# Performance work log

Hardware: AMD Instinct MI355X
Metric: run time of the kernel (lower is better)

The kernel has to match this reference:

```python
import jax, jax.numpy as jnp
import numpy as np
from math import sqrt


def _build_transitions(dim):
    # Upper-triangular (i<=j) pairs in the same row-major order as the torch loop.
    iu0, iu1 = np.triu_indices(dim)
    n_mono = len(iu0)
    idx = np.arange(n_mono)
    M = np.zeros((dim, dim), dtype=np.int32)
    M[iu0, iu1] = idx
    M[iu1, iu0] = idx
    coef_trans = np.full((n_mono, 1), sqrt(2.0), dtype=np.float32)
    coef_trans[idx[iu0 == iu1]] = 1.0  # diagonal coefficients stay scale 1
    return iu0, iu1, M.reshape(-1), coef_trans


def setup_inputs() -> dict:
    key = jax.random.key(0)
    k1, k2, k3, k4 = jax.random.split(key, 4)
    dim, n_quadrics, B = 512, 64, 2048
    n_mono = dim * (dim - 1) // 2 + dim  # 131328
    points = jax.random.normal(k1, (B, dim), dtype=jnp.float32)
    # orthogonal-ish init is only an init detail; random normal keeps math identical
    q_coefs = jax.random.normal(k2, (n_mono, n_quadrics), dtype=jnp.float32) / np.sqrt(n_mono)
    l_coefs = 2.0 * jax.random.uniform(k3, (dim, n_quadrics), dtype=jnp.float32) - 1.0
    free_coefs = 2.0 * jax.random.uniform(k4, (1, n_quadrics), dtype=jnp.float32) - 1.0
    return {"points": points, "q_coefs": q_coefs, "l_coefs": l_coefs, "free_coefs": free_coefs}


def reference(points, q_coefs, l_coefs, free_coefs):
    B, dim = points.shape
    nq = q_coefs.shape[1]
    iu0, iu1, inds_trans, coef_trans_np = _build_transitions(dim)
    coef_trans = jnp.asarray(coef_trans_np)

    # quadratic monomials: q[b, k] = p[b, i_k] * p[b, j_k]  (upper-tri order)
    q = points[:, iu0] * points[:, iu1]  # (B, n_mono)

    coefs = q_coefs * coef_trans  # (n_mono, nq) real coefficients

    # values of quadrics at points
    values = jnp.abs(q @ coefs + points @ l_coefs + free_coefs)  # (B, nq)

    # symmetric full matrices gathered from flat coefficient vector
    m_full = coefs[inds_trans].reshape(dim, dim, nq)  # (dim, dim, nq)
    dm = (jnp.eye(dim, dtype=points.dtype) + 1.0)[:, :, None]  # 2 on diag, ... wait: eye+ones -> 2 diag, 1 off
    m_scaled = m_full * dm

    # gradients: grad[b, k, e] = sum_d p[b, d] * m_scaled[d, e, k] + l_coefs[e, k]
    q_grad = jnp.einsum("bd,dek->bke", points, m_scaled) + l_coefs.T[None, :, :]  # (B, nq, dim)
    grad = jnp.sum(q_grad * q_grad, axis=2)  # (B, nq)

    norm = jnp.linalg.norm(q_coefs, axis=0)  # (nq,)
    scores = (jnp.sqrt(grad / 4.0 + values * norm) - jnp.sqrt(grad) / 2.0) / norm
    return scores
```

## Files before the change

### kernel.cpp

```cpp
#include <hip/hip_runtime.h>

#define DIM 512
#define NQ 64
#define BATCH 2048

typedef __bf16  bf16x8  __attribute__((ext_vector_type(8)));
typedef float   floatx4 __attribute__((ext_vector_type(4)));

static __device__ inline unsigned short f2bf(float f) {
    unsigned int u = __float_as_uint(f);
    return (unsigned short)((u + 0x7fffu + ((u >> 16) & 1u)) >> 16);
}
static __device__ inline float bf2f(unsigned short h) {
    return __uint_as_float((unsigned int)h << 16);
}
static __device__ inline unsigned int pack2(float a, float b) {
    return (unsigned)f2bf(a) | ((unsigned)f2bf(b) << 16);
}

__global__ void hsq_pack_kernel(const float* __restrict__ pts,
                                unsigned short* __restrict__ Pb) {
    const int i8 = blockIdx.x * 256 + threadIdx.x;
    const float4 v1 = *(const float4*)(pts + (size_t)i8 * 8);
    const float4 v2 = *(const float4*)(pts + (size_t)i8 * 8 + 4);
    uint4 wv;
    wv.x = pack2(v1.x, v1.y); wv.y = pack2(v1.z, v1.w);
    wv.z = pack2(v2.x, v2.y); wv.w = pack2(v2.z, v2.w);
    *(uint4*)(Pb + (size_t)i8 * 8) = wv;
}

__global__ __launch_bounds__(256, 4)
void hsq_expand_kernel(const float* __restrict__ qc,
                       unsigned short* __restrict__ W,
                       float* __restrict__ npart) {
    const int e    = blockIdx.x;
    const int dblk = blockIdx.y;
    const int pb   = blockIdx.y * 512 + blockIdx.x;
    const int wid  = threadIdx.x >> 6;
    const int k    = threadIdx.x & 63;
    const int d0   = dblk * 128 + wid * 32;

    __shared__ unsigned short tv[64 * 136];
    __shared__ float part[4][64];

    float v[32];
#pragma unroll
    for (int s = 0; s < 32; ++s) {
        const int d = d0 + s;
        const int i = d < e ? d : e;
        const int j = d < e ? e : d;
        const int idx = i * DIM - ((i * (i - 1)) >> 1) + (j - i);
        v[s] = qc[(size_t)idx * NQ + k];
    }

    float nacc = 0.0f;
#pragma unroll
    for (int s = 0; s < 32; ++s)
        if (d0 + s >= e) nacc += v[s] * v[s];

#pragma unroll
    for (int t = 0; t < 4; ++t) {
        float sc[8];
#pragma unroll
        for (int q = 0; q < 8; ++q) {
            const int d = d0 + t * 8 + q;
            sc[q] = v[t * 8 + q] * ((d == e) ? 2.0f : 1.41421356237309515f);
        }
        uint4 w;
        w.x = pack2(sc[0], sc[1]); w.y = pack2(sc[2], sc[3]);
        w.z = pack2(sc[4], sc[5]); w.w = pack2(sc[6], sc[7]);
        *(uint4*)&tv[k * 136 + wid * 32 + t * 8] = w;
    }
    part[wid][k] = nacc;
    __syncthreads();

#pragma unroll
    for (int r = 0; r < 4; ++r) {
        const int kk = r * 16 + (threadIdx.x >> 4);
        const int u  = threadIdx.x & 15;
        const uint4 w = *(const uint4*)&tv[kk * 136 + u * 8];
        *(uint4*)(W + ((size_t)(kk * DIM + e)) * DIM + dblk * 128 + u * 8) = w;
    }
    if (threadIdx.x < 64) {
        npart[(size_t)k * 2048 + pb] =
            part[0][k] + part[1][k] + part[2][k] + part[3][k];
    }
}

__global__ __launch_bounds__(512, 2)
void hsq_gemm_kernel(const unsigned short* __restrict__ Pb,
                     const unsigned short* __restrict__ W,
                     const float* __restrict__ l_coefs,
                     float2* __restrict__ part) {
    extern __shared__ unsigned short smem[];

    const int bid = blockIdx.x;
    const int wg  = (bid & 7) * 128 + (bid >> 3);
    const int k   = wg >> 4;
    const int rem = wg & 15;
    const int et  = rem >> 3;
    const int mt  = rem & 7;
    const int m0  = mt * 256;

    const int tid  = threadIdx.x;
    const int lane = tid & 63;
    const int w    = tid >> 6;
    const int wm   = w >> 2;
    const int wn   = w & 3;
    const int c    = lane & 15;
    const int quad = lane >> 4;

    const unsigned short* Wk = W + ((size_t)k * DIM + (size_t)et * 256) * DIM;

    const int scolb = ((tid & 7) * 16) ^ (((tid >> 3) & 7) << 4);
    const unsigned short* pAs = Pb + (size_t)(m0 + (tid >> 3)) * DIM + (scolb >> 1);
    const unsigned short* pBs = Wk + (size_t)(tid >> 3) * DIM + (scolb >> 1);

    const int xorv  = (c & 7) << 4;
    const int koff0 = ((0 * 64 + quad * 16) ^ xorv) >> 1;
    const int koff1 = ((1 * 64 + quad * 16) ^ xorv) >> 1;
    const int awoff = wm * 8192 + c * 64;
    const int bwoff = (wn >> 1) * 8192 + (wn & 1) * 4096 + c * 64;

#define STAGE_HALF(LDSELEM, GSRC) do {                                         \
    _Pragma("unroll")                                                          \
    for (int cc_ = 0; cc_ < 2; ++cc_) {                                        \
        __builtin_amdgcn_global_load_lds(                                      \
            (const __attribute__((address_space(1))) unsigned int*)            \
                ((GSRC) + (size_t)(cc_ * 64) * DIM),                           \
            (__attribute__((address_space(3))) unsigned int*)                  \
                (smem + (LDSELEM) + cc_ * 4096 + tid * 8),                     \
            16, 0, 0);                                                         \
    }                                                                          \
} while (0)

#define LOADB(BBASE) do {                                                      \
    _Pragma("unroll")                                                          \
    for (int ni_ = 0; ni_ < 4; ++ni_) {                                        \
        bfr[ni_][0] = *(const bf16x8*)(smem + (BBASE) + bwoff + ni_ * 1024 + koff0); \
        bfr[ni_][1] = *(const bf16x8*)(smem + (BBASE) + bwoff + ni_ * 1024 + koff1); \
    }                                                                          \
} while (0)

#define PHASE(ABASE, MI0, PRE_B, STAGE_AND_WAIT) do {                          \
    bf16x8 a00 = *(const bf16x8*)(smem + (ABASE) + awoff + (MI0) * 1024 + koff0);     \
    bf16x8 a01 = *(const bf16x8*)(smem + (ABASE) + awoff + (MI0) * 1024 + koff1);     \
    bf16x8 a10 = *(const bf16x8*)(smem + (ABASE) + awoff + ((MI0) + 1) * 1024 + koff0); \
    bf16x8 a11 = *(const bf16x8*)(smem + (ABASE) + awoff + ((MI0) + 1) * 1024 + koff1); \
    PRE_B;                                                                     \
    STAGE_AND_WAIT;                                                            \
    asm volatile("" ::: "memory");                                             \
    __builtin_amdgcn_s_barrier();                                              \
    asm volatile("" ::: "memory");                                             \
    __builtin_amdgcn_s_setprio(1);                                             \
    _Pragma("unroll")                                                          \
    for (int ni_ = 0; ni_ < 4; ++ni_) {                                        \
        acc[(MI0)][ni_]     = __builtin_amdgcn_mfma_f32_16x16x32_bf16(a00, bfr[ni_][0], acc[(MI0)][ni_], 0, 0, 0);     \
        acc[(MI0)][ni_]     = __builtin_amdgcn_mfma_f32_16x16x32_bf16(a01, bfr[ni_][1], acc[(MI0)][ni_], 0, 0, 0);     \
        acc[(MI0) + 1][ni_] = __builtin_amdgcn_mfma_f32_16x16x32_bf16(a10, bfr[ni_][0], acc[(MI0) + 1][ni_], 0, 0, 0); \
        acc[(MI0) + 1][ni_] = __builtin_amdgcn_mfma_f32_16x16x32_bf16(a11, bfr[ni_][1], acc[(MI0) + 1][ni_], 0, 0, 0); \
    }                                                                          \
    __builtin_amdgcn_s_setprio(0);                                             \
    asm volatile("" ::: "memory");                                             \
    __builtin_amdgcn_s_barrier();                                              \
    asm volatile("" ::: "memory");                                             \
} while (0)

    floatx4 acc[8][4];
#pragma unroll
    for (int mi = 0; mi < 8; ++mi)
#pragma unroll
        for (int ni = 0; ni < 4; ++ni)
            acc[mi][ni] = (floatx4){0.f, 0.f, 0.f, 0.f};

    bf16x8 bfr[4][2];

    STAGE_HALF(0,             pAs);
    STAGE_HALF(8192,          pAs + 128 * DIM);
    STAGE_HALF(16384,         pBs);
    STAGE_HALF(16384 + 8192,  pBs + 128 * DIM);
    STAGE_HALF(49152,         pBs + 64);
    STAGE_HALF(49152 + 8192,  pBs + 128 * DIM + 64);
    asm volatile("s_waitcnt vmcnt(4)" ::: "memory");
    __builtin_amdgcn_s_barrier();
    asm volatile("" ::: "memory");

    for (int it = 0; it < 4; ++it) {
        const unsigned short* pA1 = pAs + (size_t)(2 * it + 1) * 64;
        const unsigned short* pB2 = pBs + (size_t)(2 * it + 2) * 64;
        const unsigned short* pA2 = pAs + (size_t)(2 * it + 2) * 64;
        const unsigned short* pB3 = pBs + (size_t)(2 * it + 3) * 64;

        PHASE(0, 0, LOADB(16384), { STAGE_HALF(32768, pA1); });
        PHASE(0, 2, ((void)0),    { STAGE_HALF(32768 + 8192, pA1 + 128 * DIM); });
        PHASE(0, 4, ((void)0),    { if (it < 3) STAGE_HALF(16384, pB2); });
        PHASE(0, 6, ((void)0), {
            if (it < 3) {
                STAGE_HALF(16384 + 8192, pB2 + 128 * DIM);
                asm volatile("s_waitcnt vmcnt(4)" ::: "memory");
            } else {
                asm volatile("s_waitcnt vmcnt(0)" ::: "memory");
            }
        });
        PHASE(32768, 0, LOADB(49152), { if (it < 3) STAGE_HALF(0, pA2); });
        PHASE(32768, 2, ((void)0),    { if (it < 3) STAGE_HALF(8192, pA2 + 128 * DIM); });
        PHASE(32768, 4, ((void)0),    { if (it < 3) STAGE_HALF(49152, pB3); });
        PHASE(32768, 6, ((void)0), {
            if (it < 3) {
                STAGE_HALF(49152 + 8192, pB3 + 128 * DIM);
                asm volatile("s_waitcnt vmcnt(4)" ::: "memory");
            }
        });
    }
#undef PHASE
#undef LOADB
#undef STAGE_HALF

    __syncthreads();

    float lcv[4];
#pragma unroll
    for (int ni = 0; ni < 4; ++ni)
        lcv[ni] = l_coefs[(et * 256 + wn * 64 + ni * 16 + c) * NQ + k];

    const unsigned short* Pe = Pb + (size_t)(m0 + wm * 128) * DIM + et * 256 + wn * 64 + c;
    float* red = (float*)smem;

#pragma unroll
    for (int mi = 0; mi < 8; ++mi)
#pragma unroll
        for (int r = 0; r < 4; ++r) {
            const unsigned short* Prow = Pe + (size_t)(mi * 16 + quad * 4 + r) * DIM;
            float pv = 0.f, pg = 0.f;
#pragma unroll
            for (int ni = 0; ni < 4; ++ni) {
                const float g = acc[mi][ni][r];
                const float l = lcv[ni];
                pv += bf2f(Prow[ni * 16]) * (0.5f * g + l);
                const float gq = g + l;
                pg += gq * gq;
            }
#pragma unroll
            for (int off = 1; off < 16; off <<= 1) {
                pv += __shfl_xor(pv, off);
                pg += __shfl_xor(pg, off);
            }
            if (c == 0) {
                const int row16 = mi * 16 + quad * 4 + r;
                red[(w * 128 + row16) * 2 + 0] = pv;
                red[(w * 128 + row16) * 2 + 1] = pg;
            }
        }
    __syncthreads();

    if (tid < 256) {
        const int row16 = tid & 127;
        const int wmf   = tid >> 7;
        float pv = 0.f, pg = 0.f;
#pragma unroll
        for (int wnf = 0; wnf < 4; ++wnf) {
            const int wi = wmf * 4 + wnf;
            pv += red[(wi * 128 + row16) * 2 + 0];
            pg += red[(wi * 128 + row16) * 2 + 1];
        }
        part[((size_t)(et * NQ + k)) * BATCH + m0 + wmf * 128 + row16] =
            make_float2(pv, pg);
    }
}

__global__ void hsq_final_kernel(const float2* __restrict__ part,
                                 const float* __restrict__ npart,
                                 const float* __restrict__ free_coefs,
                                 float* __restrict__ out) {
    const int k = blockIdx.x;
    const int t = threadIdx.x;
    __shared__ float ws[4];

    const float4* src = (const float4*)(npart + (size_t)k * 2048);
    const float4 a = src[t * 2], b = src[t * 2 + 1];
    float s = a.x + a.y + a.z + a.w + b.x + b.y + b.z + b.w;
#pragma unroll
    for (int off = 1; off < 64; off <<= 1) s += __shfl_xor(s, off);
    if ((t & 63) == 0) ws[t >> 6] = s;
    __syncthreads();
    const float nrm = sqrtf(ws[0] + ws[1] + ws[2] + ws[3]);
    const float fc  = free_coefs[k];

#pragma unroll
    for (int i = 0; i < 8; ++i) {
        const int bidx = i * 256 + t;
        float pv = 0.f, pg = 0.f;
#pragma unroll
        for (int eb = 0; eb < 2; ++eb) {
            const float2 p = part[((size_t)(eb * NQ + k)) * BATCH + bidx];
            pv += p.x; pg += p.y;
        }
        const float vals = fabsf(pv + fc);
        out[(size_t)bidx * NQ + k] = (sqrtf(0.25f * pg + vals * nrm) - 0.5f * sqrtf(pg)) / nrm;
    }
}

extern "C" void kernel_launch(void* const* d_in, const int* in_sizes, int n_in,
                              void* d_out, int out_size, void* d_ws, size_t ws_size,
                              hipStream_t stream) {
    const float* points     = (const float*)d_in[0];
    const float* q_coefs    = (const float*)d_in[1];
    const float* l_coefs    = (const float*)d_in[2];
    const float* free_coefs = (const float*)d_in[3];
    float* out = (float*)d_out;

    char* ws = (char*)d_ws;
    unsigned short* W  = (unsigned short*)ws;
    unsigned short* Pb = (unsigned short*)(ws + 33554432);
    float2*         part  = (float2*)(ws + 35651584);
    float*          npart = (float*)(ws + 37748736);

    static bool attr_done = false;
    if (!attr_done) {
        (void)hipFuncSetAttribute((const void*)hsq_gemm_kernel,
                                  hipFuncAttributeMaxDynamicSharedMemorySize,
                                  131072);
        attr_done = true;
    }

    hsq_pack_kernel<<<dim3(BATCH * DIM / 8 / 256), 256, 0, stream>>>(points, Pb);
    hsq_expand_kernel<<<dim3(DIM, 4), 256, 0, stream>>>(q_coefs, W, npart);
    hsq_gemm_kernel<<<dim3(1024), dim3(512), 131072, stream>>>(Pb, W, l_coefs, part);
    hsq_final_kernel<<<dim3(NQ), 256, 0, stream>>>(part, npart, free_coefs, out);
}
```

Measured before the change: 194.3 us.

## Process four quadrics per GEMM workgroup with in-loop fused epilogue

Each GEMM workgroup now loops over four consecutive quadric coefficient matrices for the same batch tile instead of one. The pipelined K loop runs 16 iterations, and the reduction epilogue runs after every fourth iteration using a separate LDS region, then resets the accumulators. The aim is to amortize prologue and epilogue costs and reduce the block count to one wave over the CUs. In exchange, the larger LDS footprint likely limits occupancy to one block per CU, and the epilogue now sits serially inside the main loop.

Measured after the change: 275.2 us. 1.42x slower.

```diff
diff --git a/kernel.cpp b/kernel.cpp
--- a/kernel.cpp
+++ b/kernel.cpp
@@ -94,13 +94,12 @@
                      float2* __restrict__ part) {
     extern __shared__ unsigned short smem[];
 
-    const int bid = blockIdx.x;
-    const int wg  = (bid & 7) * 128 + (bid >> 3);
-    const int k   = wg >> 4;
-    const int rem = wg & 15;
-    const int et  = rem >> 3;
-    const int mt  = rem & 7;
-    const int m0  = mt * 256;
+    const int bid  = blockIdx.x;
+    const int wg   = (bid & 7) * 32 + (bid >> 3);
+    const int kgrp = wg >> 4;
+    const int et   = (wg >> 3) & 1;
+    const int mt   = wg & 7;
+    const int m0   = mt * 256;
 
     const int tid  = threadIdx.x;
     const int lane = tid & 63;
@@ -110,17 +109,20 @@
     const int c    = lane & 15;
     const int quad = lane >> 4;
 
-    const unsigned short* Wk = W + ((size_t)k * DIM + (size_t)et * 256) * DIM;
-
     const int scolb = ((tid & 7) * 16) ^ (((tid >> 3) & 7) << 4);
     const unsigned short* pAs = Pb + (size_t)(m0 + (tid >> 3)) * DIM + (scolb >> 1);
-    const unsigned short* pBs = Wk + (size_t)(tid >> 3) * DIM + (scolb >> 1);
+    const unsigned short* pBs = W + (size_t)(kgrp * 4) * DIM * DIM
+                                  + (size_t)(et * 256 + (tid >> 3)) * DIM + (scolb >> 1);
+#define PA(g) (pAs + (size_t)((g) & 7) * 64)
+#define PB(g) (pBs + (size_t)((g) >> 3) * (DIM * DIM) + (size_t)((g) & 7) * 64)
 
     const int xorv  = (c & 7) << 4;
     const int koff0 = ((0 * 64 + quad * 16) ^ xorv) >> 1;
     const int koff1 = ((1 * 64 + quad * 16) ^ xorv) >> 1;
     const int awoff = wm * 8192 + c * 64;
     const int bwoff = (wn >> 1) * 8192 + (wn & 1) * 4096 + c * 64;
+
+    float* red = (float*)&smem[65536];
 
 #define STAGE_HALF(LDSELEM, GSRC) do {                                         \
     _Pragma("unroll")                                                          \
@@ -175,97 +177,105 @@
 
     bf16x8 bfr[4][2];
 
-    STAGE_HALF(0,             pAs);
-    STAGE_HALF(8192,          pAs + 128 * DIM);
-    STAGE_HALF(16384,         pBs);
-    STAGE_HALF(16384 + 8192,  pBs + 128 * DIM);
-    STAGE_HALF(49152,         pBs + 64);
-    STAGE_HALF(49152 + 8192,  pBs + 128 * DIM + 64);
+    const unsigned short* Pe = Pb + (size_t)(m0 + wm * 128) * DIM + et * 256 + wn * 64 + c;
+
+    STAGE_HALF(0,             PA(0));
+    STAGE_HALF(8192,          PA(0) + 128 * DIM);
+    STAGE_HALF(16384,         PB(0));
+    STAGE_HALF(16384 + 8192,  PB(0) + 128 * DIM);
+    STAGE_HALF(49152,         PB(1));
+    STAGE_HALF(49152 + 8192,  PB(1) + 128 * DIM);
     asm volatile("s_waitcnt vmcnt(4)" ::: "memory");
     __builtin_amdgcn_s_barrier();
     asm volatile("" ::: "memory");
 
-    for (int it = 0; it < 4; ++it) {
-        const unsigned short* pA1 = pAs + (size_t)(2 * it + 1) * 64;
-        const unsigned short* pB2 = pBs + (size_t)(2 * it + 2) * 64;
-        const unsigned short* pA2 = pAs + (size_t)(2 * it + 2) * 64;
-        const unsigned short* pB3 = pBs + (size_t)(2 * it + 3) * 64;
-
-        PHASE(0, 0, LOADB(16384), { STAGE_HALF(32768, pA1); });
-        PHASE(0, 2, ((void)0),    { STAGE_HALF(32768 + 8192, pA1 + 128 * DIM); });
-        PHASE(0, 4, ((void)0),    { if (it < 3) STAGE_HALF(16384, pB2); });
+#pragma unroll 1
+    for (int it = 0; it < 16; ++it) {
+        const int g1 = 2 * it + 1, g2 = 2 * it + 2, g3 = 2 * it + 3;
+
+        PHASE(0, 0, LOADB(16384), { STAGE_HALF(32768, PA(g1)); });
+        PHASE(0, 2, ((void)0),    { STAGE_HALF(32768 + 8192, PA(g1) + 128 * DIM); });
+        PHASE(0, 4, ((void)0),    { if (it < 15) STAGE_HALF(16384, PB(g2)); });
         PHASE(0, 6, ((void)0), {
-            if (it < 3) {
-                STAGE_HALF(16384 + 8192, pB2 + 128 * DIM);
+            if (it < 15) {
+                STAGE_HALF(16384 + 8192, PB(g2) + 128 * DIM);
                 asm volatile("s_waitcnt vmcnt(4)" ::: "memory");
             } else {
                 asm volatile("s_waitcnt vmcnt(0)" ::: "memory");
             }
         });
-        PHASE(32768, 0, LOADB(49152), { if (it < 3) STAGE_HALF(0, pA2); });
-        PHASE(32768, 2, ((void)0),    { if (it < 3) STAGE_HALF(8192, pA2 + 128 * DIM); });
-        PHASE(32768, 4, ((void)0),    { if (it < 3) STAGE_HALF(49152, pB3); });
+        PHASE(32768, 0, LOADB(49152), { if (it < 15) STAGE_HALF(0, PA(g2)); });
+        PHASE(32768, 2, ((void)0),    { if (it < 15) STAGE_HALF(8192, PA(g2) + 128 * DIM); });
+        PHASE(32768, 4, ((void)0),    { if (it < 15) STAGE_HALF(49152, PB(g3)); });
         PHASE(32768, 6, ((void)0), {
-            if (it < 3) {
-                STAGE_HALF(49152 + 8192, pB3 + 128 * DIM);
+            if (it < 15) {
+                STAGE_HALF(49152 + 8192, PB(g3) + 128 * DIM);
                 asm volatile("s_waitcnt vmcnt(4)" ::: "memory");
             }
         });
+
+        if ((it & 3) == 3) {
+            const int kk = kgrp * 4 + (it >> 2);
+            float lcv[4];
+#pragma unroll
+            for (int ni = 0; ni < 4; ++ni)
+                lcv[ni] = l_coefs[(et * 256 + wn * 64 + ni * 16 + c) * NQ + kk];
+
+#pragma unroll
+            for (int mi = 0; mi < 8; ++mi)
+#pragma unroll
+                for (int r = 0; r < 4; ++r) {
+                    const unsigned short* Prow =
+                        Pe + (size_t)(mi * 16 + quad * 4 + r) * DIM;
+                    float pv = 0.f, pg = 0.f;
+#pragma unroll
+                    for (int ni = 0; ni < 4; ++ni) {
+                        const float g = acc[mi][ni][r];
+                        const float l = lcv[ni];
+                        pv += bf2f(Prow[ni * 16]) * (0.5f * g + l);
+                        const float gq = g + l;
+                        pg += gq * gq;
+                    }
+#pragma unroll
+                    for (int off = 1; off < 16; off <<= 1) {
+                        pv += __shfl_xor(pv, off);
+                        pg += __shfl_xor(pg, off);
+                    }
+                    if (c == 0) {
+                        const int row16 = mi * 16 + quad * 4 + r;
+                        red[(w * 128 + row16) * 2 + 0] = pv;
+                        red[(w * 128 + row16) * 2 + 1] = pg;
+                    }
+                }
+            asm volatile("s_waitcnt lgkmcnt(0)" ::: "memory");
+            __builtin_amdgcn_s_barrier();
+            asm volatile("" ::: "memory");
+
+            if (tid < 256) {
+                const int row16 = tid & 127;
+                const int wmf   = tid >> 7;
+                float pv = 0.f, pg = 0.f;
+#pragma unroll
+                for (int wnf = 0; wnf < 4; ++wnf) {
+                    const int wi = wmf * 4 + wnf;
+                    pv += red[(wi * 128 + row16) * 2 + 0];
+                    pg += red[(wi * 128 + row16) * 2 + 1];
+                }
+                part[((size_t)(et * NQ + kk)) * BATCH + m0 + wmf * 128 + row16] =
+                    make_float2(pv, pg);
+            }
+#pragma unroll
+            for (int mi = 0; mi < 8; ++mi)
+#pragma unroll
+                for (int ni = 0; ni < 4; ++ni)
+                    acc[mi][ni] = (floatx4){0.f, 0.f, 0.f, 0.f};
+        }
     }
 #undef PHASE
 #undef LOADB
 #undef STAGE_HALF
-
-    __syncthreads();
-
-    float lcv[4];
-#pragma unroll
-    for (int ni = 0; ni < 4; ++ni)
-        lcv[ni] = l_coefs[(et * 256 + wn * 64 + ni * 16 + c) * NQ + k];
-
-    const unsigned short* Pe = Pb + (size_t)(m0 + wm * 128) * DIM + et * 256 + wn * 64 + c;
-    float* red = (float*)smem;
-
-#pragma unroll
-    for (int mi = 0; mi < 8; ++mi)
-#pragma unroll
-        for (int r = 0; r < 4; ++r) {
-            const unsigned short* Prow = Pe + (size_t)(mi * 16 + quad * 4 + r) * DIM;
-            float pv = 0.f, pg = 0.f;
-#pragma unroll
-            for (int ni = 0; ni < 4; ++ni) {
-                const float g = acc[mi][ni][r];
-                const float l = lcv[ni];
-                pv += bf2f(Prow[ni * 16]) * (0.5f * g + l);
-                const float gq = g + l;
-                pg += gq * gq;
-            }
-#pragma unroll
-            for (int off = 1; off < 16; off <<= 1) {
-                pv += __shfl_xor(pv, off);
-                pg += __shfl_xor(pg, off);
-            }
-            if (c == 0) {
-                const int row16 = mi * 16 + quad * 4 + r;
-                red[(w * 128 + row16) * 2 + 0] = pv;
-                red[(w * 128 + row16) * 2 + 1] = pg;
-            }
-        }
-    __syncthreads();
-
-    if (tid < 256) {
-        const int row16 = tid & 127;
-        const int wmf   = tid >> 7;
-        float pv = 0.f, pg = 0.f;
-#pragma unroll
-        for (int wnf = 0; wnf < 4; ++wnf) {
-            const int wi = wmf * 4 + wnf;
-            pv += red[(wi * 128 + row16) * 2 + 0];
-            pg += red[(wi * 128 + row16) * 2 + 1];
-        }
-        part[((size_t)(et * NQ + k)) * BATCH + m0 + wmf * 128 + row16] =
-            make_float2(pv, pg);
-    }
+#undef PA
+#undef PB
 }
 
 __global__ void hsq_final_kernel(const float2* __restrict__ part,
@@ -319,12 +329,12 @@
     if (!attr_done) {
         (void)hipFuncSetAttribute((const void*)hsq_gemm_kernel,
                                   hipFuncAttributeMaxDynamicSharedMemorySize,
-                                  131072);
+                                  139264);
         attr_done = true;
     }
 
     hsq_pack_kernel<<<dim3(BATCH * DIM / 8 / 256), 256, 0, stream>>>(points, Pb);
     hsq_expand_kernel<<<dim3(DIM, 4), 256, 0, stream>>>(q_coefs, W, npart);
-    hsq_gemm_kernel<<<dim3(1024), dim3(512), 131072, stream>>>(Pb, W, l_coefs, part);
+    hsq_gemm_kernel<<<dim3(256), dim3(512), 139264, stream>>>(Pb, W, l_coefs, part);
     hsq_final_kernel<<<dim3(NQ), 256, 0, stream>>>(part, npart, free_coefs, out);
 }
```
